# Performance work log

Hardware: AMD Instinct MI355X
Metric: run time of the kernel (lower is better)

The kernel has to match this reference:

```python
import jax, jax.numpy as jnp
import numpy as np

HEADS = 8
H_DIM = 64
SCALE = H_DIM ** -0.5


def setup_inputs() -> dict:
    key = jax.random.key(0)
    ks = jax.random.split(key, 10)
    B, Q, K, D = 4, 2048, 2048, 512
    hidden = HEADS * H_DIM  # 512
    s = 0.02  # weight init scale
    return {
        "q": jax.random.normal(ks[0], (B, Q, D), jnp.float32),
        "k": jax.random.normal(ks[1], (B, K, D), jnp.float32),
        "v": jax.random.normal(ks[2], (B, K, D), jnp.float32),
        "bias": jax.random.normal(ks[3], (B, Q, K), jnp.float32),
        "Wq": jax.random.normal(ks[4], (D, hidden), jnp.float32) * s,
        "bq": jnp.zeros((hidden,), jnp.float32),
        "Wk": jax.random.normal(ks[5], (D, hidden), jnp.float32) * s,
        "bk": jnp.zeros((hidden,), jnp.float32),
        "Wv": jax.random.normal(ks[6], (D, hidden), jnp.float32) * s,
        "bv": jnp.zeros((hidden,), jnp.float32),
        "Wg": jax.random.normal(ks[7], (D, hidden), jnp.float32) * s,
        "bg": jnp.zeros((hidden,), jnp.float32),
        "Wo": jax.random.normal(ks[8], (hidden, D), jnp.float32) * s,
        "bo": jnp.zeros((D,), jnp.float32),
    }


def reference(q, k, v, bias, Wq, bq, Wk, bk, Wv, bv, Wg, bg, Wo, bo):
    B, Q, _ = q.shape
    K = k.shape[-2]
    wq = (q @ Wq + bq).reshape(B, Q, HEADS, H_DIM) * SCALE   # (B,Q,H,Dh)
    wk = (k @ Wk + bk).reshape(B, K, HEADS, H_DIM)           # (B,K,H,Dh)
    wv = (v @ Wv + bv).reshape(B, K, HEADS, H_DIM)           # (B,K,H,Dh)
    # scores (B,Q,K,H); softmax over k_len axis (-2), matching torch softmax(-2)
    scores = jnp.einsum("bqhd,bkhd->bqkh", wq, wk)
    a = jax.nn.softmax(scores, axis=-2)
    # bias added AFTER softmax, broadcast over heads -- faithful to source
    a = a + bias[..., None]
    o = jnp.einsum("bqkh,bkhd->bqhd", a, wv).reshape(B, Q, HEADS * H_DIM)
    g = jax.nn.sigmoid(q @ Wg + bg)
    o = g * o
    return o @ Wo + bo
```

## Files before the change

### kernel.cpp

```cpp
#include <hip/hip_runtime.h>
#include <hip/hip_bf16.h>

#define NB 4
#define SEQ 2048
#define DMODEL 512
#define HEADS 8
#define HDIM 64
#define QKS_L2E 0.18033688011112042f

typedef __bf16 bf16_t;
typedef bf16_t bf16x8 __attribute__((ext_vector_type(8)));
typedef bf16_t bf16x4 __attribute__((ext_vector_type(4)));
typedef float f32x4 __attribute__((ext_vector_type(4)));

__device__ __forceinline__ int swz(int row, int c16) {
    return (row << 7) + (((c16) ^ (row & 7)) << 4);
}

__device__ __forceinline__ bf16x4 cvt4(float4 v) {
    bf16x4 r;
    r[0] = (bf16_t)v.x; r[1] = (bf16_t)v.y; r[2] = (bf16_t)v.z; r[3] = (bf16_t)v.w;
    return r;
}

__global__ __launch_bounds__(256) void prep_weights(
    const float* __restrict__ Wq, const float* __restrict__ Wg,
    const float* __restrict__ Wk, const float* __restrict__ Wv,
    const float* __restrict__ Wo, bf16_t* __restrict__ out)
{
    __shared__ float t[64][65];
    const int m  = blockIdx.x >> 6;
    const int t2 = blockIdx.x & 63;
    const int tr = t2 >> 3, tc = t2 & 7;
    const float* W = (m == 0) ? Wq : (m == 1) ? Wg : (m == 2) ? Wk : (m == 3) ? Wv : Wo;
    const int r0 = threadIdx.x >> 6;
    const int c  = threadIdx.x & 63;
#pragma unroll
    for (int i = 0; i < 64; i += 4) {
        int row = i + r0;
        t[row][c] = W[(size_t)(tr * 64 + row) * DMODEL + tc * 64 + c];
    }
    __syncthreads();
    bf16_t* o = out + (size_t)m * (DMODEL * DMODEL);
#pragma unroll
    for (int i = 0; i < 64; i += 4) {
        int row = i + r0;
        o[(size_t)(tc * 64 + row) * DMODEL + tr * 64 + c] = (bf16_t)t[c][row];
    }
}

template <int MODE>
__global__ __launch_bounds__(512) void proj_gemm(
    const float* __restrict__ A, const bf16_t* __restrict__ Wt,
    const float* __restrict__ bias0, const float* __restrict__ bias1,
    bf16_t* __restrict__ out0, bf16_t* __restrict__ out1)
{
    constexpr int NT = (MODE == 0) ? 8 : 4;
    __shared__ __align__(16) char smA[16384];
    __shared__ __align__(16) char smB[16384];
    const int tid = threadIdx.x;
    const int lane = tid & 63, w = tid >> 6;
    const int nt = blockIdx.x & (NT - 1);
    const int mt = blockIdx.x / NT;
    const int m0 = mt << 7, n0 = nt << 7;
    const int wr = w >> 2, wc = w & 3;
    const int lr = lane & 15, lg = lane >> 4;

    f32x4 acc[4][2] = {};
    for (int kb = 0; kb < 8; ++kb) {
        const int k0 = kb * 64;
        __syncthreads();
#pragma unroll
        for (int i = 0; i < 4; ++i) {
            int f = tid + i * 512;
            int row = f >> 4, c4 = f & 15;
            float4 v = *(const float4*)(A + (size_t)(m0 + row) * DMODEL + k0 + c4 * 4);
            *(bf16x4*)(smA + swz(row, c4 >> 1) + ((c4 & 1) << 3)) = cvt4(v);
        }
#pragma unroll
        for (int i = 0; i < 2; ++i) {
            int f = tid + i * 512;
            int row = f >> 3, c16 = f & 7;
            uint4 v = *(const uint4*)(Wt + (size_t)(n0 + row) * DMODEL + k0 + c16 * 8);
            *(uint4*)(smB + swz(row, c16)) = v;
        }
        __syncthreads();
#pragma unroll
        for (int ks = 0; ks < 2; ++ks) {
            bf16x8 a[4], bb[2];
#pragma unroll
            for (int mi = 0; mi < 4; ++mi)
                a[mi] = *(const bf16x8*)(smA + swz(wr * 64 + mi * 16 + lr, lg + ks * 4));
#pragma unroll
            for (int ni = 0; ni < 2; ++ni)
                bb[ni] = *(const bf16x8*)(smB + swz(wc * 32 + ni * 16 + lr, lg + ks * 4));
#pragma unroll
            for (int mi = 0; mi < 4; ++mi)
#pragma unroll
                for (int ni = 0; ni < 2; ++ni)
                    acc[mi][ni] = __builtin_amdgcn_mfma_f32_16x16x32_bf16(a[mi], bb[ni], acc[mi][ni], 0, 0, 0);
        }
    }
#pragma unroll
    for (int mi = 0; mi < 4; ++mi) {
#pragma unroll
        for (int ni = 0; ni < 2; ++ni) {
            const int col = n0 + wc * 32 + ni * 16 + lr;
            const int row0 = m0 + wr * 64 + mi * 16 + lg * 4;
            if (MODE == 0) {
                const bool isG = col >= DMODEL;
                const int c = isG ? col - DMODEL : col;
                const float bb = isG ? bias1[c] : bias0[c];
#pragma unroll
                for (int j = 0; j < 4; ++j) {
                    float x = acc[mi][ni][j] + bb;
                    bf16_t r = isG ? (bf16_t)(1.0f / (1.0f + __expf(-x)))
                                   : (bf16_t)(x * QKS_L2E);
                    (isG ? out1 : out0)[(size_t)(row0 + j) * DMODEL + c] = r;
                }
            } else if (MODE == 1) {
                const float bb = bias0[col];
#pragma unroll
                for (int j = 0; j < 4; ++j)
                    out0[(size_t)(row0 + j) * DMODEL + col] = (bf16_t)(acc[mi][ni][j] + bb);
            } else {
                const float bb = bias0[col];
                const int b = row0 >> 11, key = row0 & (SEQ - 1);
                const int h = col >> 6, d = col & 63;
                bf16x4 r;
#pragma unroll
                for (int j = 0; j < 4; ++j) r[j] = (bf16_t)(acc[mi][ni][j] + bb);
                *(bf16x4*)(out0 + ((size_t)(b * HEADS + h) * HDIM + d) * SEQ + key) = r;
            }
        }
    }
}

__global__ __launch_bounds__(256) void attn_kernel(
    const bf16_t* __restrict__ wq, const bf16_t* __restrict__ wk,
    const bf16_t* __restrict__ wvt, bf16_t* __restrict__ attn_o)
{
    __shared__ __align__(16) char smK[8192];
    __shared__ __align__(16) char smV[8192];
    __shared__ __align__(16) char smP[8192];
    const int tid = threadIdx.x;
    const int lane = tid & 63, w = tid >> 6;
    const int bh = blockIdx.x & 31;
    const int qt = blockIdx.x >> 5;
    const int b = bh >> 3, h = bh & 7;
    const int q0 = qt << 6;
    const int lr = lane & 15, lg = lane >> 4;

    bf16x8 qf[2];
    {
        int row = q0 + w * 16 + lr;
        const bf16_t* p = wq + (size_t)(b * SEQ + row) * DMODEL + h * HDIM + lg * 8;
        qf[0] = *(const bf16x8*)(p);
        qf[1] = *(const bf16x8*)(p + 32);
    }
    const bf16_t* kbase = wk + (size_t)b * SEQ * DMODEL + h * HDIM;
    const bf16_t* vbase = wvt + (size_t)(b * HEADS + h) * HDIM * SEQ;
    const int srow0 = tid >> 3,         sc0 = tid & 7;
    const int srow1 = (tid + 256) >> 3, sc1 = (tid + 256) & 7;

    float lsum[4] = {0.f, 0.f, 0.f, 0.f};
    f32x4 oacc[4] = {};

    for (int kt = 0; kt < SEQ / 64; ++kt) {
        const int k0 = kt * 64;
        __syncthreads();
        {
            uint4 vk0 = *(const uint4*)(kbase + (size_t)(k0 + srow0) * DMODEL + sc0 * 8);
            uint4 vk1 = *(const uint4*)(kbase + (size_t)(k0 + srow1) * DMODEL + sc1 * 8);
            uint4 vv0 = *(const uint4*)(vbase + (size_t)srow0 * SEQ + k0 + sc0 * 8);
            uint4 vv1 = *(const uint4*)(vbase + (size_t)srow1 * SEQ + k0 + sc1 * 8);
            *(uint4*)(smK + swz(srow0, sc0)) = vk0;
            *(uint4*)(smK + swz(srow1, sc1)) = vk1;
            *(uint4*)(smV + swz(srow0, sc0)) = vv0;
            *(uint4*)(smV + swz(srow1, sc1)) = vv1;
        }
        __syncthreads();

        f32x4 s[4] = {};
#pragma unroll
        for (int ks = 0; ks < 2; ++ks) {
#pragma unroll
            for (int nf = 0; nf < 4; ++nf) {
                bf16x8 kbf = *(const bf16x8*)(smK + swz(nf * 16 + lr, lg + ks * 4));
                s[nf] = __builtin_amdgcn_mfma_f32_16x16x32_bf16(qf[ks], kbf, s[nf], 0, 0, 0);
            }
        }
#pragma unroll
        for (int nf = 0; nf < 4; ++nf) {
#pragma unroll
            for (int j = 0; j < 4; ++j) {
                float p = __builtin_amdgcn_exp2f(s[nf][j]);
                s[nf][j] = p;
                lsum[j] += p;
            }
        }
        char* pbase = smP + w * 2048;
#pragma unroll
        for (int nf = 0; nf < 4; ++nf) {
            int col = nf * 16 + lr;
#pragma unroll
            for (int j = 0; j < 4; ++j) {
                int row = lg * 4 + j;
                *(bf16_t*)(pbase + swz(row, col >> 3) + ((col & 7) << 1)) = (bf16_t)s[nf][j];
            }
        }
#pragma unroll
        for (int ks = 0; ks < 2; ++ks) {
            bf16x8 pa = *(const bf16x8*)(pbase + swz(lr, lg + ks * 4));
#pragma unroll
            for (int nf = 0; nf < 4; ++nf) {
                bf16x8 vb = *(const bf16x8*)(smV + swz(nf * 16 + lr, lg + ks * 4));
                oacc[nf] = __builtin_amdgcn_mfma_f32_16x16x32_bf16(pa, vb, oacc[nf], 0, 0, 0);
            }
        }
    }
    float rinv[4];
#pragma unroll
    for (int j = 0; j < 4; ++j) {
        float t = lsum[j];
#pragma unroll
        for (int off = 1; off < 16; off <<= 1) t += __shfl_xor(t, off);
        rinv[j] = 1.0f / t;
    }
#pragma unroll
    for (int nf = 0; nf < 4; ++nf) {
        int col = h * HDIM + nf * 16 + lr;
#pragma unroll
        for (int j = 0; j < 4; ++j) {
            int row = q0 + w * 16 + lg * 4 + j;
            attn_o[(size_t)(b * SEQ + row) * DMODEL + col] = (bf16_t)(oacc[nf][j] * rinv[j]);
        }
    }
}

__global__ __launch_bounds__(512) void biasv_gemm(
    const float* __restrict__ bias, const bf16_t* __restrict__ wvt,
    float* __restrict__ Bv)
{
    __shared__ __align__(16) char smA[16384];
    __shared__ __align__(16) char smB[16384];
    const int tid = threadIdx.x;
    const int lane = tid & 63, w = tid >> 6;
    const int nt = blockIdx.x & 3;
    const int mt = (blockIdx.x >> 2) & 15;
    const int b = blockIdx.x >> 6;
    const int m0 = mt << 7, n0 = nt << 7;
    const int wr = w >> 2, wc = w & 3;
    const int lr = lane & 15, lg = lane >> 4;

    f32x4 acc[4][2] = {};
    for (int kb = 0; kb < SEQ / 64; ++kb) {
        const int k0 = kb * 64;
        __syncthreads();
#pragma unroll
        for (int i = 0; i < 4; ++i) {
            int f = tid + i * 512;
            int row = f >> 4, c4 = f & 15;
            float4 v = *(const float4*)(bias + ((size_t)b * SEQ + m0 + row) * SEQ + k0 + c4 * 4);
            *(bf16x4*)(smA + swz(row, c4 >> 1) + ((c4 & 1) << 3)) = cvt4(v);
        }
#pragma unroll
        for (int i = 0; i < 2; ++i) {
            int f = tid + i * 512;
            int row = f >> 3, c16 = f & 7;
            int n = n0 + row;
            uint4 v = *(const uint4*)(wvt + ((size_t)(b * HEADS + (n >> 6)) * HDIM + (n & 63)) * SEQ + k0 + c16 * 8);
            *(uint4*)(smB + swz(row, c16)) = v;
        }
        __syncthreads();
#pragma unroll
        for (int ks = 0; ks < 2; ++ks) {
            bf16x8 a[4], bb[2];
#pragma unroll
            for (int mi = 0; mi < 4; ++mi)
                a[mi] = *(const bf16x8*)(smA + swz(wr * 64 + mi * 16 + lr, lg + ks * 4));
#pragma unroll
            for (int ni = 0; ni < 2; ++ni)
                bb[ni] = *(const bf16x8*)(smB + swz(wc * 32 + ni * 16 + lr, lg + ks * 4));
#pragma unroll
            for (int mi = 0; mi < 4; ++mi)
#pragma unroll
                for (int ni = 0; ni < 2; ++ni)
                    acc[mi][ni] = __builtin_amdgcn_mfma_f32_16x16x32_bf16(a[mi], bb[ni], acc[mi][ni], 0, 0, 0);
        }
    }
#pragma unroll
    for (int mi = 0; mi < 4; ++mi) {
#pragma unroll
        for (int ni = 0; ni < 2; ++ni) {
            int col = n0 + wc * 32 + ni * 16 + lr;
#pragma unroll
            for (int j = 0; j < 4; ++j) {
                int row = m0 + wr * 64 + mi * 16 + lg * 4 + j;
                Bv[((size_t)b * SEQ + row) * DMODEL + col] = acc[mi][ni][j];
            }
        }
    }
}

__global__ __launch_bounds__(512) void out_gemm(
    const bf16_t* __restrict__ atn, const float* __restrict__ Bvp,
    const bf16_t* __restrict__ gg, const bf16_t* __restrict__ Wot,
    const float* __restrict__ bo, float* __restrict__ out)
{
    __shared__ __align__(16) char smA[16384];
    __shared__ __align__(16) char smB[16384];
    const int tid = threadIdx.x;
    const int lane = tid & 63, w = tid >> 6;
    const int nt = blockIdx.x & 3;
    const int mt = blockIdx.x >> 2;
    const int m0 = mt << 7, n0 = nt << 7;
    const int wr = w >> 2, wc = w & 3;
    const int lr = lane & 15, lg = lane >> 4;

    f32x4 acc[4][2] = {};
    for (int kb = 0; kb < 8; ++kb) {
        const int k0 = kb * 64;
        __syncthreads();
#pragma unroll
        for (int i = 0; i < 2; ++i) {
            int f = tid + i * 512;
            int row = f >> 3, c8 = f & 7;
            size_t idx = (size_t)(m0 + row) * DMODEL + k0 + c8 * 8;
            bf16x8 a8 = *(const bf16x8*)(atn + idx);
            bf16x8 g8 = *(const bf16x8*)(gg + idx);
            float4 blo = *(const float4*)(Bvp + idx);
            float4 bhi = *(const float4*)(Bvp + idx + 4);
            bf16x8 r;
            r[0] = (bf16_t)((float)g8[0] * ((float)a8[0] + blo.x));
            r[1] = (bf16_t)((float)g8[1] * ((float)a8[1] + blo.y));
            r[2] = (bf16_t)((float)g8[2] * ((float)a8[2] + blo.z));
            r[3] = (bf16_t)((float)g8[3] * ((float)a8[3] + blo.w));
            r[4] = (bf16_t)((float)g8[4] * ((float)a8[4] + bhi.x));
            r[5] = (bf16_t)((float)g8[5] * ((float)a8[5] + bhi.y));
            r[6] = (bf16_t)((float)g8[6] * ((float)a8[6] + bhi.z));
            r[7] = (bf16_t)((float)g8[7] * ((float)a8[7] + bhi.w));
            *(bf16x8*)(smA + swz(row, c8)) = r;
        }
#pragma unroll
        for (int i = 0; i < 2; ++i) {
            int f = tid + i * 512;
            int row = f >> 3, c16 = f & 7;
            uint4 v = *(const uint4*)(Wot + (size_t)(n0 + row) * DMODEL + k0 + c16 * 8);
            *(uint4*)(smB + swz(row, c16)) = v;
        }
        __syncthreads();
#pragma unroll
        for (int ks = 0; ks < 2; ++ks) {
            bf16x8 a[4], bb[2];
#pragma unroll
            for (int mi = 0; mi < 4; ++mi)
                a[mi] = *(const bf16x8*)(smA + swz(wr * 64 + mi * 16 + lr, lg + ks * 4));
#pragma unroll
            for (int ni = 0; ni < 2; ++ni)
                bb[ni] = *(const bf16x8*)(smB + swz(wc * 32 + ni * 16 + lr, lg + ks * 4));
#pragma unroll
            for (int mi = 0; mi < 4; ++mi)
#pragma unroll
                for (int ni = 0; ni < 2; ++ni)
                    acc[mi][ni] = __builtin_amdgcn_mfma_f32_16x16x32_bf16(a[mi], bb[ni], acc[mi][ni], 0, 0, 0);
        }
    }
#pragma unroll
    for (int mi = 0; mi < 4; ++mi) {
#pragma unroll
        for (int ni = 0; ni < 2; ++ni) {
            int col = n0 + wc * 32 + ni * 16 + lr;
            float bb = bo[col];
#pragma unroll
            for (int j = 0; j < 4; ++j) {
                int row = m0 + wr * 64 + mi * 16 + lg * 4 + j;
                out[(size_t)row * DMODEL + col] = acc[mi][ni][j] + bb;
            }
        }
    }
}

extern "C" void kernel_launch(void* const* d_in, const int* in_sizes, int n_in,
                              void* d_out, int out_size, void* d_ws, size_t ws_size,
                              hipStream_t stream)
{
    const float* q    = (const float*)d_in[0];
    const float* k    = (const float*)d_in[1];
    const float* v    = (const float*)d_in[2];
    const float* bias = (const float*)d_in[3];
    const float* Wq   = (const float*)d_in[4];
    const float* bq   = (const float*)d_in[5];
    const float* Wk   = (const float*)d_in[6];
    const float* bk   = (const float*)d_in[7];
    const float* Wv   = (const float*)d_in[8];
    const float* bv   = (const float*)d_in[9];
    const float* Wg   = (const float*)d_in[10];
    const float* bg   = (const float*)d_in[11];
    const float* Wo   = (const float*)d_in[12];
    const float* bo   = (const float*)d_in[13];
    float* out = (float*)d_out;

    char* ws = (char*)d_ws;
    const size_t WSZ = (size_t)DMODEL * DMODEL;
    const size_t TOK = (size_t)NB * SEQ * DMODEL;
    bf16_t* Wt   = (bf16_t*)ws;
    bf16_t* wq_  = (bf16_t*)(ws + 5 * WSZ * 2);
    bf16_t* wk_  = wq_ + TOK;
    bf16_t* wvt  = wk_ + TOK;
    bf16_t* atn  = wvt + TOK;
    bf16_t* g_   = atn + TOK;
    float*  Bv_  = (float*)(g_ + TOK);

    prep_weights<<<320, 256, 0, stream>>>(Wq, Wg, Wk, Wv, Wo, Wt);
    proj_gemm<0><<<512, 512, 0, stream>>>(q, Wt,           bq, bg,      wq_, g_);
    proj_gemm<1><<<256, 512, 0, stream>>>(k, Wt + 2 * WSZ, bk, nullptr, wk_, nullptr);
    proj_gemm<2><<<256, 512, 0, stream>>>(v, Wt + 3 * WSZ, bv, nullptr, wvt, nullptr);
    attn_kernel<<<1024, 256, 0, stream>>>(wq_, wk_, wvt, atn);
    biasv_gemm<<<256, 512, 0, stream>>>(bias, wvt, Bv_);
    out_gemm<<<256, 512, 0, stream>>>(atn, Bv_, g_, Wt + 4 * WSZ, bo, out);
}
```

Measured before the change: 408.2 us.

## Double-buffer biasv_gemm with direct global-to-LDS loads and block swizzle

```diff
diff --git a/kernel.cpp b/kernel.cpp
--- a/kernel.cpp
+++ b/kernel.cpp
@@ -21,6 +21,12 @@
     bf16x4 r;
     r[0] = (bf16_t)v.x; r[1] = (bf16_t)v.y; r[2] = (bf16_t)v.z; r[3] = (bf16_t)v.w;
     return r;
+}
+
+__device__ __forceinline__ void gl_lds16(const void* g, void* lds) {
+    __builtin_amdgcn_global_load_lds(
+        (const __attribute__((address_space(1))) void*)g,
+        (__attribute__((address_space(3))) void*)lds, 16, 0, 0);
 }
 
 __global__ __launch_bounds__(256) void prep_weights(
@@ -242,52 +248,81 @@
     const float* __restrict__ bias, const bf16_t* __restrict__ wvt,
     float* __restrict__ Bv)
 {
-    __shared__ __align__(16) char smA[16384];
-    __shared__ __align__(16) char smB[16384];
+    __shared__ __align__(16) char sm[98304];
     const int tid = threadIdx.x;
     const int lane = tid & 63, w = tid >> 6;
-    const int nt = blockIdx.x & 3;
-    const int mt = (blockIdx.x >> 2) & 15;
-    const int b = blockIdx.x >> 6;
+    const int bid = (int)blockIdx.x;
+    const int swzb = (bid & 7) * 32 + (bid >> 3);
+    const int nt = swzb & 3;
+    const int mt = (swzb >> 2) & 15;
+    const int b  = swzb >> 6;
     const int m0 = mt << 7, n0 = nt << 7;
     const int wr = w >> 2, wc = w & 3;
     const int lr = lane & 15, lg = lane >> 4;
 
+    const float*  Asrc = bias + ((size_t)b * SEQ + m0) * SEQ;
+    const bf16_t* Bsrc = wvt + ((size_t)b * DMODEL + n0) * SEQ;
+
+    const int aLr = lane >> 4;
+    const int aS  = lane & 15;
+    const int bLr = lane >> 3;
+    const int bC16 = (lane & 7) ^ bLr;
+
+    auto STAGE = [&](int kb, char* bufA, char* bufB) {
+        const int k0 = kb * 64;
+#pragma unroll
+        for (int i = 0; i < 4; ++i) {
+            const int c = (w << 2) + i;
+            const int row = (c << 2) + aLr;
+            const int sc = aS ^ (row & 15);
+            gl_lds16(Asrc + (size_t)row * SEQ + k0 + sc * 4, bufA + (c << 10));
+        }
+#pragma unroll
+        for (int i = 0; i < 2; ++i) {
+            const int c = (w << 1) + i;
+            const int row = (c << 3) + bLr;
+            gl_lds16(Bsrc + (size_t)row * SEQ + k0 + bC16 * 8, bufB + (c << 10));
+        }
+    };
+
     f32x4 acc[4][2] = {};
+    STAGE(0, sm, sm + 32768);
+    __syncthreads();
+    int cur = 0;
     for (int kb = 0; kb < SEQ / 64; ++kb) {
-        const int k0 = kb * 64;
-        __syncthreads();
-#pragma unroll
-        for (int i = 0; i < 4; ++i) {
-            int f = tid + i * 512;
-            int row = f >> 4, c4 = f & 15;
-            float4 v = *(const float4*)(bias + ((size_t)b * SEQ + m0 + row) * SEQ + k0 + c4 * 4);
-            *(bf16x4*)(smA + swz(row, c4 >> 1) + ((c4 & 1) << 3)) = cvt4(v);
-        }
-#pragma unroll
-        for (int i = 0; i < 2; ++i) {
-            int f = tid + i * 512;
-            int row = f >> 3, c16 = f & 7;
-            int n = n0 + row;
-            uint4 v = *(const uint4*)(wvt + ((size_t)(b * HEADS + (n >> 6)) * HDIM + (n & 63)) * SEQ + k0 + c16 * 8);
-            *(uint4*)(smB + swz(row, c16)) = v;
-        }
-        __syncthreads();
+        const int coff = cur * 49152;
+        char* curA = sm + coff;
+        char* curB = sm + 32768 + coff;
+        if (kb + 1 < SEQ / 64) {
+            const int noff = 49152 - coff;
+            STAGE(kb + 1, sm + noff, sm + 32768 + noff);
+        }
 #pragma unroll
         for (int ks = 0; ks < 2; ++ks) {
             bf16x8 a[4], bb[2];
 #pragma unroll
-            for (int mi = 0; mi < 4; ++mi)
-                a[mi] = *(const bf16x8*)(smA + swz(wr * 64 + mi * 16 + lr, lg + ks * 4));
+            for (int mi = 0; mi < 4; ++mi) {
+                const int row = wr * 64 + mi * 16 + lr;
+                const int kk = lg + ks * 4;
+                const char* rbase = curA + (row << 8);
+                float4 lo = *(const float4*)(rbase + (((kk * 2)     ^ lr) << 4));
+                float4 hi = *(const float4*)(rbase + (((kk * 2 + 1) ^ lr) << 4));
+                bf16x8 av;
+                av[0] = (bf16_t)lo.x; av[1] = (bf16_t)lo.y; av[2] = (bf16_t)lo.z; av[3] = (bf16_t)lo.w;
+                av[4] = (bf16_t)hi.x; av[5] = (bf16_t)hi.y; av[6] = (bf16_t)hi.z; av[7] = (bf16_t)hi.w;
+                a[mi] = av;
+            }
 #pragma unroll
             for (int ni = 0; ni < 2; ++ni)
-                bb[ni] = *(const bf16x8*)(smB + swz(wc * 32 + ni * 16 + lr, lg + ks * 4));
+                bb[ni] = *(const bf16x8*)(curB + swz(wc * 32 + ni * 16 + lr, lg + ks * 4));
 #pragma unroll
             for (int mi = 0; mi < 4; ++mi)
 #pragma unroll
                 for (int ni = 0; ni < 2; ++ni)
                     acc[mi][ni] = __builtin_amdgcn_mfma_f32_16x16x32_bf16(a[mi], bb[ni], acc[mi][ni], 0, 0, 0);
         }
+        __syncthreads();
+        cur ^= 1;
     }
 #pragma unroll
     for (int mi = 0; mi < 4; ++mi) {
```

Measured after the change: 387.7 us. 1.05x faster.
